# Kernel optimization log

Measured on AMD Instinct MI355X. Metric: run time of the kernel, lower is better.

The kernel has to match this reference:

```python
import jax, jax.numpy as jnp
import numpy as np
import math

HIDDEN = 2048
HEADS = 16
HEAD_DIM = HIDDEN // HEADS
RANK = HIDDEN // 2  # rank_ratio=0.5
B, S = 1, 4096


def setup_inputs() -> dict:
    key = jax.random.key(0)
    ks = jax.random.split(key, 10)
    sd = lambda fan_in: 1.0 / math.sqrt(fan_in)
    inp = {
        "hidden_states": jax.random.normal(ks[0], (B, S, HIDDEN), dtype=jnp.float32),
        "attention_mask": jnp.zeros((B, 1, S, S), dtype=jnp.float32),
        # low-rank projection weights; Linear weight shape is [out, in]
        "q_V": jax.random.uniform(ks[1], (RANK, HIDDEN), jnp.float32, -sd(HIDDEN), sd(HIDDEN)),
        "q_U": jax.random.uniform(ks[2], (HIDDEN, RANK), jnp.float32, -sd(RANK), sd(RANK)),
        "k_V": jax.random.uniform(ks[3], (RANK, HIDDEN), jnp.float32, -sd(HIDDEN), sd(HIDDEN)),
        "k_U": jax.random.uniform(ks[4], (HIDDEN, RANK), jnp.float32, -sd(RANK), sd(RANK)),
        "v_V": jax.random.uniform(ks[5], (RANK, HIDDEN), jnp.float32, -sd(HIDDEN), sd(HIDDEN)),
        "v_U": jax.random.uniform(ks[6], (HIDDEN, RANK), jnp.float32, -sd(RANK), sd(RANK)),
        "o_W": jax.random.uniform(ks[7], (HIDDEN, HIDDEN), jnp.float32, -sd(HIDDEN), sd(HIDDEN)),
        "o_b": jax.random.uniform(ks[8], (HIDDEN,), jnp.float32, -sd(HIDDEN), sd(HIDDEN)),
    }
    return inp


def _split_heads(x):
    # [B,S,HIDDEN] -> [B,H,S,Dh]
    b, s, _ = x.shape
    return x.reshape(b, s, HEADS, HEAD_DIM).transpose(0, 2, 1, 3)


def reference(hidden_states, attention_mask, q_V, q_U, k_V, k_U, v_V, v_U, o_W, o_b):
    # low-rank QKV: x @ V^T @ U^T
    q = _split_heads((hidden_states @ q_V.T) @ q_U.T)
    k = _split_heads((hidden_states @ k_V.T) @ k_U.T)
    v = _split_heads((hidden_states @ v_V.T) @ v_U.T)
    scores = jnp.einsum("bhqd,bhkd->bhqk", q, k) / math.sqrt(HEAD_DIM)
    scores = scores + attention_mask
    attn = jax.nn.softmax(scores, axis=-1)
    out = jnp.einsum("bhqk,bhkd->bhqd", attn, v)
    out = out.transpose(0, 2, 1, 3).reshape(hidden_states.shape[0], hidden_states.shape[1], HIDDEN)
    out = out @ o_W.T + o_b
    return out
```

## Files before the change

### kernel.cpp

```cpp
#include <hip/hip_runtime.h>

#define HIDDEN 2048
#define HEADS 16
#define HD 128
#define RANK 1024
#define SEQ 4096

typedef __bf16 bf16_t;
typedef __bf16 bf16x8 __attribute__((ext_vector_type(8)));
typedef __bf16 bf16x4 __attribute__((ext_vector_type(4)));
typedef float f32x4 __attribute__((ext_vector_type(4)));

#define MFMA_BF16(a, b, c) __builtin_amdgcn_mfma_f32_16x16x32_bf16((a), (b), (c), 0, 0, 0)

__device__ __forceinline__ void gload16(const bf16_t* g, bf16_t* l) {
  __builtin_amdgcn_global_load_lds(
      (const __attribute__((address_space(1))) unsigned int*)g,
      (__attribute__((address_space(3))) unsigned int*)l, 16, 0, 0);
}

struct CastSeg { const float* s; bf16_t* d; int n4; };
struct CastArgs { CastSeg seg[8]; };

__global__ __launch_bounds__(256) void cast_bf16_kernel(CastArgs a) {
  const int stride = gridDim.x * blockDim.x;
  const int tid0 = blockIdx.x * blockDim.x + threadIdx.x;
#pragma unroll
  for (int i = 0; i < 8; i++) {
    const float4* src = (const float4*)a.seg[i].s;
    bf16x4* dst = (bf16x4*)a.seg[i].d;
    const int n4 = a.seg[i].n4;
    for (int j = tid0; j < n4; j += stride) {
      float4 v = src[j];
      dst[j] = bf16x4{(bf16_t)v.x, (bf16_t)v.y, (bf16_t)v.z, (bf16_t)v.w};
    }
  }
}

template <int OUT_MODE>
__global__ __launch_bounds__(256) void gemm3(const bf16_t* __restrict__ A, int lda, int aOff,
                                             const bf16_t* __restrict__ W0,
                                             const bf16_t* __restrict__ W1,
                                             const bf16_t* __restrict__ W2,
                                             int nPerThird, int K,
                                             void* __restrict__ Cp, int ldc, size_t cOff,
                                             const float* __restrict__ bias, float s0,
                                             bf16_t* __restrict__ Ct) {
  __shared__ bf16_t As[128 * 32];
  __shared__ bf16_t Bs[128 * 32];
  const int tid = threadIdx.x, lane = tid & 63, wave = tid >> 6;
  const int wr = wave >> 1, wc = wave & 1, quad = lane >> 4, l15 = lane & 15;

  const int gx = gridDim.x, nwg = gx * gridDim.y;
  const int orig = blockIdx.x + gx * blockIdx.y;
  const int wgid = (orig & 7) * (nwg >> 3) + (orig >> 3);
  const int bx = wgid % gx, by = wgid / gx;

  const int n0g = bx * 128;
  const int third = n0g / nPerThird;
  const int n0 = n0g - third * nPerThird;
  const bf16_t* W = third == 0 ? W0 : (third == 1 ? W1 : W2);
  const bf16_t* Ab = A + (size_t)third * aOff;
  const int m0 = by * 128;
  const float sc = (third == 0) ? s0 : 1.f;

  f32x4 acc[4][4];
#pragma unroll
  for (int i = 0; i < 4; i++)
#pragma unroll
    for (int j = 0; j < 4; j++) acc[i][j] = f32x4{0.f, 0.f, 0.f, 0.f};

  const int KT = K >> 5;
  for (int kt = 0; kt < KT; ++kt) {
#pragma unroll
    for (int i = 0; i < 2; i++) {
      int slot = (wave * 2 + i) * 64 + lane;
      int row = slot >> 2, cp = slot & 3;
      int cl = cp ^ ((row >> 1) & 3);
      gload16(Ab + (size_t)(m0 + row) * lda + kt * 32 + cl * 8, As + (size_t)(wave * 2 + i) * 512);
    }
#pragma unroll
    for (int i = 0; i < 2; i++) {
      int slot = (wave * 2 + i) * 64 + lane;
      int row = slot >> 2, cp = slot & 3;
      int cl = cp ^ ((row >> 1) & 3);
      gload16(W + (size_t)(n0 + row) * K + kt * 32 + cl * 8, Bs + (size_t)(wave * 2 + i) * 512);
    }
    __syncthreads();

    bf16x8 af[4], bfr[4];
#pragma unroll
    for (int mt = 0; mt < 4; mt++) {
      int row = wr * 64 + mt * 16 + l15;
      int phys = quad ^ ((row >> 1) & 3);
      af[mt] = *reinterpret_cast<const bf16x8*>(As + row * 32 + phys * 8);
    }
#pragma unroll
    for (int nt = 0; nt < 4; nt++) {
      int row = wc * 64 + nt * 16 + l15;
      int phys = quad ^ ((row >> 1) & 3);
      bfr[nt] = *reinterpret_cast<const bf16x8*>(Bs + row * 32 + phys * 8);
    }
#pragma unroll
    for (int mt = 0; mt < 4; mt++)
#pragma unroll
      for (int nt = 0; nt < 4; nt++) acc[mt][nt] = MFMA_BF16(af[mt], bfr[nt], acc[mt][nt]);
    __syncthreads();
  }

  if constexpr (OUT_MODE == 2) {
    if (third == 2) {
#pragma unroll
      for (int nt = 0; nt < 4; nt++) {
        int col = n0 + wc * 64 + nt * 16 + l15;
#pragma unroll
        for (int mt = 0; mt < 4; mt++) {
          int rowb = m0 + wr * 64 + mt * 16 + quad * 4;
          bf16x4 tv = {(bf16_t)acc[mt][nt][0], (bf16_t)acc[mt][nt][1],
                       (bf16_t)acc[mt][nt][2], (bf16_t)acc[mt][nt][3]};
          *reinterpret_cast<bf16x4*>(Ct + (size_t)col * SEQ + rowb) = tv;
        }
      }
      return;
    }
  }

#pragma unroll
  for (int nt = 0; nt < 4; nt++) {
    int col = n0 + wc * 64 + nt * 16 + l15;
    float bv = 0.f;
    if constexpr (OUT_MODE == 1) bv = bias[col];
#pragma unroll
    for (int mt = 0; mt < 4; mt++) {
      int rowb = m0 + wr * 64 + mt * 16 + quad * 4;
#pragma unroll
      for (int r = 0; r < 4; r++) {
        float vx = acc[mt][nt][r];
        if constexpr (OUT_MODE == 1)
          ((float*)Cp + (size_t)third * cOff)[(size_t)(rowb + r) * ldc + col] = vx + bv;
        else
          ((bf16_t*)Cp + (size_t)third * cOff)[(size_t)(rowb + r) * ldc + col] = (bf16_t)(vx * sc);
      }
    }
  }
}

__global__ __launch_bounds__(256, 2) void attn_kernel(const bf16_t* __restrict__ qb,
                                                      const bf16_t* __restrict__ kb,
                                                      const bf16_t* __restrict__ vtp,
                                                      const float* __restrict__ mask,
                                                      bf16_t* __restrict__ ao) {
  __shared__ bf16_t Ks[2][64 * 128];
  __shared__ bf16_t Vs[3][128 * 64];
  const int tid = threadIdx.x, lane = tid & 63, w = tid >> 6;
  const int quad = lane >> 4, l15 = lane & 15;
  const int head = blockIdx.x, q0 = blockIdx.y * 128;
  const float LOG2E = 1.4426950408889634f;
  const int NT = SEQ / 64;

  bf16x8 qf[2][4];
#pragma unroll
  for (int qt = 0; qt < 2; qt++)
#pragma unroll
    for (int ks = 0; ks < 4; ks++)
      qf[qt][ks] = *reinterpret_cast<const bf16x8*>(
          qb + (size_t)(q0 + w * 32 + qt * 16 + l15) * HIDDEN + head * HD + ks * 32 + quad * 8);

  f32x4 O[8][2];
#pragma unroll
  for (int dt = 0; dt < 8; dt++)
#pragma unroll
    for (int qt = 0; qt < 2; qt++) O[dt][qt] = f32x4{0.f, 0.f, 0.f, 0.f};
  float lacc[2] = {0.f, 0.f};

  auto stageK = [&](int kt, int buf) {
#pragma unroll
    for (int i = 0; i < 4; i++) {
      int slot = (w * 4 + i) * 64 + lane;
      int row = slot >> 4, cp = slot & 15;
      int cl = cp ^ ((row & 3) | ((row & 8) >> 1));
      gload16(kb + (size_t)(kt * 64 + row) * HIDDEN + head * HD + cl * 8,
              &Ks[buf][(size_t)(w * 4 + i) * 512]);
    }
  };
  auto stageV = [&](int kt, int buf) {
#pragma unroll
    for (int i = 0; i < 4; i++) {
      int slot = (w * 4 + i) * 64 + lane;
      int row = slot >> 3, cp = slot & 7;
      int cl = cp ^ (row & 7);
      gload16(vtp + (size_t)(head * HD + row) * SEQ + kt * 64 + cl * 8,
              &Vs[buf][(size_t)(w * 4 + i) * 512]);
    }
  };

  const int sK = (l15 & 3) | (((l15 >> 2) & 1) << 2);
  const int rA0 = ((l15 >> 2) << 3) + (l15 & 3);

  f32x4 mv[2][2][2];
  auto loadMask = [&](int kt) {
#pragma unroll
    for (int kp = 0; kp < 2; kp++)
#pragma unroll
      for (int sub = 0; sub < 2; sub++)
#pragma unroll
        for (int qt = 0; qt < 2; qt++)
          mv[kp][sub][qt] = *reinterpret_cast<const f32x4*>(
              mask + (size_t)(q0 + w * 32 + qt * 16 + l15) * SEQ + kt * 64 + kp * 32 + quad * 8 +
              sub * 4);
  };

  f32x4 sacc[2][2][2];
  bf16x8 pf[2][2];

  auto smGroup = [&](int kp, int sub) {
#pragma unroll
    for (int qt = 0; qt < 2; qt++) {
      f32x4 e;
#pragma unroll
      for (int r = 0; r < 4; r++)
        e[r] = __builtin_amdgcn_exp2f(sacc[kp][sub][qt][r] + mv[kp][sub][qt][r] * LOG2E);
      lacc[qt] += (e[0] + e[1]) + (e[2] + e[3]);
#pragma unroll
      for (int r = 0; r < 4; r++) pf[kp][qt][sub * 4 + r] = (bf16_t)e[r];
    }
  };

  auto qkT = [&](int buf) {
#pragma unroll
    for (int kp = 0; kp < 2; kp++)
#pragma unroll
      for (int sub = 0; sub < 2; sub++)
#pragma unroll
        for (int qt = 0; qt < 2; qt++) sacc[kp][sub][qt] = f32x4{0.f, 0.f, 0.f, 0.f};
#pragma unroll
    for (int ks = 0; ks < 4; ks++) {
      int phys = (ks * 4 + quad) ^ sK;
#pragma unroll
      for (int kp = 0; kp < 2; kp++)
#pragma unroll
        for (int sub = 0; sub < 2; sub++) {
          int rowA = kp * 32 + sub * 4 + rA0;
          bf16x8 ak = *reinterpret_cast<const bf16x8*>(&Ks[buf][rowA * 128 + phys * 8]);
#pragma unroll
          for (int qt = 0; qt < 2; qt++)
            sacc[kp][sub][qt] = MFMA_BF16(ak, qf[qt][ks], sacc[kp][sub][qt]);
        }
    }
  };

  auto qkT_sm = [&](int buf) {
    f32x4 ns[2][2][2];
#pragma unroll
    for (int kp = 0; kp < 2; kp++)
#pragma unroll
      for (int sub = 0; sub < 2; sub++)
#pragma unroll
        for (int qt = 0; qt < 2; qt++) ns[kp][sub][qt] = f32x4{0.f, 0.f, 0.f, 0.f};
#pragma unroll
    for (int ks = 0; ks < 4; ks++) {
      int phys = (ks * 4 + quad) ^ sK;
#pragma unroll
      for (int kp = 0; kp < 2; kp++)
#pragma unroll
        for (int sub = 0; sub < 2; sub++) {
          int rowA = kp * 32 + sub * 4 + rA0;
          bf16x8 ak = *reinterpret_cast<const bf16x8*>(&Ks[buf][rowA * 128 + phys * 8]);
#pragma unroll
          for (int qt = 0; qt < 2; qt++)
            ns[kp][sub][qt] = MFMA_BF16(ak, qf[qt][ks], ns[kp][sub][qt]);
        }
      smGroup(ks >> 1, ks & 1);
    }
#pragma unroll
    for (int kp = 0; kp < 2; kp++)
#pragma unroll
      for (int sub = 0; sub < 2; sub++)
#pragma unroll
        for (int qt = 0; qt < 2; qt++) sacc[kp][sub][qt] = ns[kp][sub][qt];
  };

  auto pv = [&](const bf16_t* Vb) {
#pragma unroll
    for (int kp = 0; kp < 2; kp++)
#pragma unroll
      for (int dt = 0; dt < 8; dt++) {
        int row = dt * 16 + l15;
        int phys = (kp * 4 + quad) ^ (l15 & 7);
        bf16x8 av = *reinterpret_cast<const bf16x8*>(&Vb[row * 64 + phys * 8]);
#pragma unroll
        for (int qt = 0; qt < 2; qt++) O[dt][qt] = MFMA_BF16(av, pf[kp][qt], O[dt][qt]);
      }
  };

  stageK(0, 0);
  stageV(0, 0);
  stageK(1, 1);
  stageV(1, 1);
  loadMask(0);
  __syncthreads();
  qkT(0);

  int vb_pv = 0;
  int vb_st = 2;
  for (int t = 0; t < NT - 1; ++t) {
    asm volatile("s_waitcnt vmcnt(8) lgkmcnt(0)" ::: "memory");
    __builtin_amdgcn_s_barrier();
    __builtin_amdgcn_sched_barrier(0);
    stageK(t + 2, t & 1);
    stageV(t + 2, vb_st);
    __builtin_amdgcn_sched_barrier(0);
    loadMask(t + 1);
    __builtin_amdgcn_s_setprio(1);
    qkT_sm((t + 1) & 1);
    pv(&Vs[vb_pv][0]);
    __builtin_amdgcn_s_setprio(0);
    vb_pv = vb_pv == 2 ? 0 : vb_pv + 1;
    vb_st = vb_st == 2 ? 0 : vb_st + 1;
  }
  smGroup(0, 0);
  smGroup(0, 1);
  smGroup(1, 0);
  smGroup(1, 1);
  pv(&Vs[vb_pv][0]);

#pragma unroll
  for (int qt = 0; qt < 2; qt++) {
    float l = lacc[qt];
    l += __shfl_xor(l, 16, 64);
    l += __shfl_xor(l, 32, 64);
    lacc[qt] = 1.f / l;
  }
#pragma unroll
  for (int dt = 0; dt < 8; dt++)
#pragma unroll
    for (int qt = 0; qt < 2; qt++) {
      int q = q0 + w * 32 + qt * 16 + l15;
      int d = head * HD + dt * 16 + quad * 4;
      f32x4 o = O[dt][qt];
      bf16x4 ov = {(bf16_t)(o[0] * lacc[qt]), (bf16_t)(o[1] * lacc[qt]),
                   (bf16_t)(o[2] * lacc[qt]), (bf16_t)(o[3] * lacc[qt])};
      *reinterpret_cast<bf16x4*>(ao + (size_t)q * HIDDEN + d) = ov;
    }
}

extern "C" void kernel_launch(void* const* d_in, const int* in_sizes, int n_in,
                              void* d_out, int out_size, void* d_ws, size_t ws_size,
                              hipStream_t stream) {
  (void)in_sizes; (void)n_in; (void)out_size; (void)ws_size;
  const float* x = (const float*)d_in[0];
  const float* mask = (const float*)d_in[1];
  const float* qV = (const float*)d_in[2];
  const float* qU = (const float*)d_in[3];
  const float* kV = (const float*)d_in[4];
  const float* kU = (const float*)d_in[5];
  const float* vV = (const float*)d_in[6];
  const float* vU = (const float*)d_in[7];
  const float* oW = (const float*)d_in[8];
  const float* ob = (const float*)d_in[9];
  float* out = (float*)d_out;

  char* ws = (char*)d_ws;
  const size_t MB = 1ull << 20;
  bf16_t* xb  = (bf16_t*)(ws);
  bf16_t* tmp = (bf16_t*)(ws + 16 * MB);
  bf16_t* qkv = (bf16_t*)(ws + 40 * MB);
  bf16_t* qVb = (bf16_t*)(ws + 88 * MB);
  bf16_t* qUb = (bf16_t*)(ws + 92 * MB);
  bf16_t* kVb = (bf16_t*)(ws + 96 * MB);
  bf16_t* kUb = (bf16_t*)(ws + 100 * MB);
  bf16_t* vVb = (bf16_t*)(ws + 104 * MB);
  bf16_t* vUb = (bf16_t*)(ws + 108 * MB);
  bf16_t* oWb = (bf16_t*)(ws + 112 * MB);
  bf16_t* vt = qkv + 2 * (size_t)SEQ * HIDDEN;

  const float kQScale = 0.088388347648318447f * 1.4426950408889634f;

  CastArgs ca;
  ca.seg[0] = {x, xb, SEQ * HIDDEN / 4};
  ca.seg[1] = {qV, qVb, RANK * HIDDEN / 4};
  ca.seg[2] = {qU, qUb, HIDDEN * RANK / 4};
  ca.seg[3] = {kV, kVb, RANK * HIDDEN / 4};
  ca.seg[4] = {kU, kUb, HIDDEN * RANK / 4};
  ca.seg[5] = {vV, vVb, RANK * HIDDEN / 4};
  ca.seg[6] = {vU, vUb, HIDDEN * RANK / 4};
  ca.seg[7] = {oW, oWb, HIDDEN * HIDDEN / 4};
  cast_bf16_kernel<<<2048, 256, 0, stream>>>(ca);

  gemm3<0><<<dim3(24, 32), 256, 0, stream>>>(xb, HIDDEN, 0, qVb, kVb, vVb, RANK, HIDDEN,
                                             tmp, 3 * RANK, (size_t)RANK, nullptr, 1.f, nullptr);
  gemm3<2><<<dim3(48, 32), 256, 0, stream>>>(tmp, 3 * RANK, RANK, qUb, kUb, vUb, HIDDEN, RANK,
                                             qkv, HIDDEN, (size_t)SEQ * HIDDEN, nullptr,
                                             kQScale, vt);
  attn_kernel<<<dim3(HEADS, SEQ / 128), 256, 0, stream>>>(qkv, qkv + (size_t)SEQ * HIDDEN, vt,
                                                          mask, xb);
  gemm3<1><<<dim3(16, 32), 256, 0, stream>>>(xb, HIDDEN, 0, oWb, oWb, oWb, HIDDEN, HIDDEN,
                                             out, HIDDEN, 0, ob, 1.f, nullptr);
}
```

Before: 550.5 us.

## Double GEMM K-tile to 64 and restructure attention loop mask prefetch

The projection GEMM now stages 64-wide K slices instead of 32, with an 8-way XOR swizzle, which halves the number of barrier pairs per GEMM while doubling shared memory per block. In the attention loop, the mask for the next tile is loaded into a separate register set and copied over after compute, and the hand-tuned vmcnt wait with raw barrier is replaced by a plain __syncthreads. The larger tile may lower occupancy, and the full __syncthreads waits on all outstanding loads, which removes the overlap the partial vmcnt wait gave.

```diff
diff --git a/kernel.cpp b/kernel.cpp
--- a/kernel.cpp
+++ b/kernel.cpp
@@ -46,8 +46,8 @@
                                              void* __restrict__ Cp, int ldc, size_t cOff,
                                              const float* __restrict__ bias, float s0,
                                              bf16_t* __restrict__ Ct) {
-  __shared__ bf16_t As[128 * 32];
-  __shared__ bf16_t Bs[128 * 32];
+  __shared__ bf16_t As[128 * 64];
+  __shared__ bf16_t Bs[128 * 64];
   const int tid = threadIdx.x, lane = tid & 63, wave = tid >> 6;
   const int wr = wave >> 1, wc = wave & 1, quad = lane >> 4, l15 = lane & 15;
 
@@ -70,41 +70,44 @@
 #pragma unroll
     for (int j = 0; j < 4; j++) acc[i][j] = f32x4{0.f, 0.f, 0.f, 0.f};
 
-  const int KT = K >> 5;
+  const int KT = K >> 6;
   for (int kt = 0; kt < KT; ++kt) {
 #pragma unroll
-    for (int i = 0; i < 2; i++) {
-      int slot = (wave * 2 + i) * 64 + lane;
-      int row = slot >> 2, cp = slot & 3;
-      int cl = cp ^ ((row >> 1) & 3);
-      gload16(Ab + (size_t)(m0 + row) * lda + kt * 32 + cl * 8, As + (size_t)(wave * 2 + i) * 512);
-    }
-#pragma unroll
-    for (int i = 0; i < 2; i++) {
-      int slot = (wave * 2 + i) * 64 + lane;
-      int row = slot >> 2, cp = slot & 3;
-      int cl = cp ^ ((row >> 1) & 3);
-      gload16(W + (size_t)(n0 + row) * K + kt * 32 + cl * 8, Bs + (size_t)(wave * 2 + i) * 512);
+    for (int i = 0; i < 4; i++) {
+      int slot = (wave * 4 + i) * 64 + lane;
+      int row = slot >> 3, cp = slot & 7;
+      int cl = cp ^ (row & 7);
+      gload16(Ab + (size_t)(m0 + row) * lda + kt * 64 + cl * 8, As + (size_t)(wave * 4 + i) * 512);
+    }
+#pragma unroll
+    for (int i = 0; i < 4; i++) {
+      int slot = (wave * 4 + i) * 64 + lane;
+      int row = slot >> 3, cp = slot & 7;
+      int cl = cp ^ (row & 7);
+      gload16(W + (size_t)(n0 + row) * K + kt * 64 + cl * 8, Bs + (size_t)(wave * 4 + i) * 512);
     }
     __syncthreads();
 
-    bf16x8 af[4], bfr[4];
-#pragma unroll
-    for (int mt = 0; mt < 4; mt++) {
-      int row = wr * 64 + mt * 16 + l15;
-      int phys = quad ^ ((row >> 1) & 3);
-      af[mt] = *reinterpret_cast<const bf16x8*>(As + row * 32 + phys * 8);
-    }
-#pragma unroll
-    for (int nt = 0; nt < 4; nt++) {
-      int row = wc * 64 + nt * 16 + l15;
-      int phys = quad ^ ((row >> 1) & 3);
-      bfr[nt] = *reinterpret_cast<const bf16x8*>(Bs + row * 32 + phys * 8);
-    }
-#pragma unroll
-    for (int mt = 0; mt < 4; mt++)
-#pragma unroll
-      for (int nt = 0; nt < 4; nt++) acc[mt][nt] = MFMA_BF16(af[mt], bfr[nt], acc[mt][nt]);
+#pragma unroll
+    for (int kk = 0; kk < 2; kk++) {
+      bf16x8 af[4], bfr[4];
+#pragma unroll
+      for (int mt = 0; mt < 4; mt++) {
+        int row = wr * 64 + mt * 16 + l15;
+        int phys = (kk * 4 + quad) ^ (l15 & 7);
+        af[mt] = *reinterpret_cast<const bf16x8*>(As + row * 64 + phys * 8);
+      }
+#pragma unroll
+      for (int nt = 0; nt < 4; nt++) {
+        int row = wc * 64 + nt * 16 + l15;
+        int phys = (kk * 4 + quad) ^ (l15 & 7);
+        bfr[nt] = *reinterpret_cast<const bf16x8*>(Bs + row * 64 + phys * 8);
+      }
+#pragma unroll
+      for (int mt = 0; mt < 4; mt++)
+#pragma unroll
+        for (int nt = 0; nt < 4; nt++) acc[mt][nt] = MFMA_BF16(af[mt], bfr[nt], acc[mt][nt]);
+    }
     __syncthreads();
   }
 
@@ -198,14 +201,15 @@
   const int rA0 = ((l15 >> 2) << 3) + (l15 & 3);
 
   f32x4 mv[2][2][2];
-  auto loadMask = [&](int kt) {
+  f32x4 nmv[2][2][2];
+  auto loadMaskTo = [&](int kt, f32x4 (&dst)[2][2][2]) {
 #pragma unroll
     for (int kp = 0; kp < 2; kp++)
 #pragma unroll
       for (int sub = 0; sub < 2; sub++)
 #pragma unroll
         for (int qt = 0; qt < 2; qt++)
-          mv[kp][sub][qt] = *reinterpret_cast<const f32x4*>(
+          dst[kp][sub][qt] = *reinterpret_cast<const f32x4*>(
               mask + (size_t)(q0 + w * 32 + qt * 16 + l15) * SEQ + kt * 64 + kp * 32 + quad * 8 +
               sub * 4);
   };
@@ -297,24 +301,27 @@
   stageV(0, 0);
   stageK(1, 1);
   stageV(1, 1);
-  loadMask(0);
+  loadMaskTo(0, mv);
   __syncthreads();
   qkT(0);
 
   int vb_pv = 0;
   int vb_st = 2;
   for (int t = 0; t < NT - 1; ++t) {
-    asm volatile("s_waitcnt vmcnt(8) lgkmcnt(0)" ::: "memory");
-    __builtin_amdgcn_s_barrier();
-    __builtin_amdgcn_sched_barrier(0);
+    __syncthreads();
     stageK(t + 2, t & 1);
     stageV(t + 2, vb_st);
-    __builtin_amdgcn_sched_barrier(0);
-    loadMask(t + 1);
+    loadMaskTo(t + 1, nmv);
     __builtin_amdgcn_s_setprio(1);
     qkT_sm((t + 1) & 1);
     pv(&Vs[vb_pv][0]);
     __builtin_amdgcn_s_setprio(0);
+#pragma unroll
+    for (int kp = 0; kp < 2; kp++)
+#pragma unroll
+      for (int sub = 0; sub < 2; sub++)
+#pragma unroll
+        for (int qt = 0; qt < 2; qt++) mv[kp][sub][qt] = nmv[kp][sub][qt];
     vb_pv = vb_pv == 2 ? 0 : vb_pv + 1;
     vb_st = vb_st == 2 ? 0 : vb_st + 1;
   }
```

After: 662.5 us. 1.2x slower.

## Double-buffer LDS tiles in gemm3 to overlap global loads with MFMA

Applied to the files above, without the earlier changes.

Splits the A and W shared-memory tiles into two buffers. The next k-tile is issued via global_load_lds before computing on the current one, and the per-iteration barriers drop from two to one. The goal is to hide global-to-LDS latency behind the MFMA work in the projection GEMMs, at the cost of doubling LDS use per block, which may lower occupancy.

```diff
diff --git a/kernel.cpp b/kernel.cpp
--- a/kernel.cpp
+++ b/kernel.cpp
@@ -46,8 +46,8 @@
                                              void* __restrict__ Cp, int ldc, size_t cOff,
                                              const float* __restrict__ bias, float s0,
                                              bf16_t* __restrict__ Ct) {
-  __shared__ bf16_t As[128 * 32];
-  __shared__ bf16_t Bs[128 * 32];
+  __shared__ bf16_t As[2][128 * 32];
+  __shared__ bf16_t Bs[2][128 * 32];
   const int tid = threadIdx.x, lane = tid & 63, wave = tid >> 6;
   const int wr = wave >> 1, wc = wave & 1, quad = lane >> 4, l15 = lane & 15;
 
@@ -70,43 +70,57 @@
 #pragma unroll
     for (int j = 0; j < 4; j++) acc[i][j] = f32x4{0.f, 0.f, 0.f, 0.f};
 
-  const int KT = K >> 5;
-  for (int kt = 0; kt < KT; ++kt) {
+  auto stage = [&](int kt, int buf) {
 #pragma unroll
     for (int i = 0; i < 2; i++) {
       int slot = (wave * 2 + i) * 64 + lane;
       int row = slot >> 2, cp = slot & 3;
       int cl = cp ^ ((row >> 1) & 3);
-      gload16(Ab + (size_t)(m0 + row) * lda + kt * 32 + cl * 8, As + (size_t)(wave * 2 + i) * 512);
+      gload16(Ab + (size_t)(m0 + row) * lda + kt * 32 + cl * 8,
+              As[buf] + (size_t)(wave * 2 + i) * 512);
     }
 #pragma unroll
     for (int i = 0; i < 2; i++) {
       int slot = (wave * 2 + i) * 64 + lane;
       int row = slot >> 2, cp = slot & 3;
       int cl = cp ^ ((row >> 1) & 3);
-      gload16(W + (size_t)(n0 + row) * K + kt * 32 + cl * 8, Bs + (size_t)(wave * 2 + i) * 512);
-    }
-    __syncthreads();
-
+      gload16(W + (size_t)(n0 + row) * K + kt * 32 + cl * 8,
+              Bs[buf] + (size_t)(wave * 2 + i) * 512);
+    }
+  };
+
+  auto compute = [&](int buf) {
     bf16x8 af[4], bfr[4];
 #pragma unroll
     for (int mt = 0; mt < 4; mt++) {
       int row = wr * 64 + mt * 16 + l15;
       int phys = quad ^ ((row >> 1) & 3);
-      af[mt] = *reinterpret_cast<const bf16x8*>(As + row * 32 + phys * 8);
+      af[mt] = *reinterpret_cast<const bf16x8*>(As[buf] + row * 32 + phys * 8);
     }
 #pragma unroll
     for (int nt = 0; nt < 4; nt++) {
       int row = wc * 64 + nt * 16 + l15;
       int phys = quad ^ ((row >> 1) & 3);
-      bfr[nt] = *reinterpret_cast<const bf16x8*>(Bs + row * 32 + phys * 8);
+      bfr[nt] = *reinterpret_cast<const bf16x8*>(Bs[buf] + row * 32 + phys * 8);
     }
 #pragma unroll
     for (int mt = 0; mt < 4; mt++)
 #pragma unroll
       for (int nt = 0; nt < 4; nt++) acc[mt][nt] = MFMA_BF16(af[mt], bfr[nt], acc[mt][nt]);
-    __syncthreads();
-  }
+  };
+
+  const int KT = K >> 5;
+  stage(0, 0);
+  for (int kt = 0; kt < KT - 1; ++kt) {
+    asm volatile("s_waitcnt vmcnt(0) lgkmcnt(0)" ::: "memory");
+    __builtin_amdgcn_s_barrier();
+    __builtin_amdgcn_sched_barrier(0);
+    stage(kt + 1, (kt + 1) & 1);
+    compute(kt & 1);
+  }
+  asm volatile("s_waitcnt vmcnt(0) lgkmcnt(0)" ::: "memory");
+  __builtin_amdgcn_s_barrier();
+  compute((KT - 1) & 1);
 
   if constexpr (OUT_MODE == 2) {
     if (third == 2) {
```

Result: faster. 537.4 us (-2.4%).
